# Optimization experiments

Measured on AMD Instinct MI355X. Metric: run time of the kernel, lower is better.

The kernel has to match this reference:

```python
import jax, jax.numpy as jnp
import numpy as np

B = 65536
G = 9          # grid_size
C = 10         # num_classes
BS = 3         # block_size = sqrt(grid_size)
CONSTRAINT_WEIGHT = 0.1


def setup_inputs() -> dict:
    key = jax.random.key(0)
    k1, k2, k3 = jax.random.split(key, 3)
    logits = jax.random.normal(k1, (B, G, G, C), dtype=jnp.float32)
    targets = jax.random.randint(k2, (B, G, G), 0, C)
    puzzles = jax.random.randint(k3, (B, G, G), 0, C)
    return {"logits": logits, "targets": targets, "puzzles": puzzles}


def _sudoku_loss(logits, targets, puzzles):
    mask = (puzzles == 0).astype(logits.dtype)               # [B, G, G]

    # --- masked cross-entropy over empty cells ---
    logp = jax.nn.log_softmax(logits, axis=-1)               # [B, G, G, C]
    ce = -jnp.take_along_axis(logp, targets[..., None], axis=-1)[..., 0]
    ce_loss = (ce * mask).sum() / (mask.sum() + 1e-8)

    # --- constraint loss (rows, cols, 3x3 boxes), fully vectorized ---
    probs = jnp.exp(logp)                                    # softmax probs
    wp = probs * mask[..., None]                             # [B, G, G, C]

    def group_mse(digit_sums, msum):
        # digit_sums: [B, G_groups, C]; msum: [B, G_groups]
        # torch: per-group F.mse_loss over [B, C-1], summed over groups
        target = msum[..., None] / G                         # [B, Gg, 1]
        diff = digit_sums[..., 1:] - target                  # [B, Gg, C-1]
        return (diff * diff).mean(axis=(0, 2)).sum()

    # rows: sum over columns (axis 2)
    row_loss = group_mse(wp.sum(axis=2), mask.sum(axis=2))
    # cols: sum over rows (axis 1)
    col_loss = group_mse(wp.sum(axis=1), mask.sum(axis=1))
    # boxes: reshape to [B, bi, ri, bj, cj, C], sum within-box dims
    box_ds = wp.reshape(B, BS, BS, BS, BS, C).sum(axis=(2, 4)).reshape(B, G, C)
    box_ms = mask.reshape(B, BS, BS, BS, BS).sum(axis=(2, 4)).reshape(B, G)
    box_loss = group_mse(box_ds, box_ms)

    num_constraints = G * 2 + BS * BS                        # 27
    constraint_loss = (row_loss + col_loss + box_loss) / num_constraints

    # torch wraps the constraint loss in torch.tensor(...), detaching it
    total = ce_loss + CONSTRAINT_WEIGHT * jax.lax.stop_gradient(constraint_loss)
    return total, ce_loss, constraint_loss


def reference(logits, targets, puzzles):
    total, ce_loss, constraint_loss = _sudoku_loss(logits, targets, puzzles)
    return total, ce_loss, constraint_loss
```

## Files before the change

### kernel.cpp

```cpp
#include <hip/hip_runtime.h>


constexpr int kB     = 65536;
constexpr int TPB    = 512;
constexpr int NBLK   = 1024;
constexpr int PPBLK  = kB / NBLK;
constexpr int PPB_R  = 6;
constexpr int ROUNDS = (PPBLK + PPB_R - 1) / PPB_R;
constexpr int NSLOT  = 256;
constexpr int SLOT_STRIDE = 16;
constexpr int CSTRIDE = 12;

__global__ __launch_bounds__(TPB, 8) void sudoku_main(
    const float* __restrict__ logits,
    const int*   __restrict__ targets,
    const int*   __restrict__ puzzles,
    float*       __restrict__ ws)
{
    __shared__ __align__(16) float probs[TPB * CSTRIDE];
    __shared__ float red[3][TPB / 64];

    const int  tid  = threadIdx.x;
    const int  q    = tid / 81;
    const bool actq = (q < PPB_R);
    const size_t blkbase = (size_t)blockIdx.x * PPBLK * 81;

    float ce = 0.f, mcnt = 0.f, diff2 = 0.f;

    int pz_cur = 1;
    if (actq) pz_cur = puzzles[blkbase + tid];

    for (int r = 0; r < ROUNDS; ++r) {
        int pz_next = 1;
        if (r + 1 < ROUNDS) {
            const bool actn = actq && ((r + 1) * PPB_R + q < PPBLK);
            if (actn) pz_next = puzzles[blkbase + (size_t)(r + 1) * (PPB_R * 81) + tid];
        }

        const bool act = actq && (r * PPB_R + q < PPBLK);
        float wv[10];
        #pragma unroll
        for (int c = 0; c < 10; ++c) wv[c] = 0.f;

        if (act && pz_cur == 0) {
            const size_t idx = blkbase + (size_t)r * (PPB_R * 81) + tid;
            const int tg = targets[idx];
            const float* xp = logits + idx * 10;
            float2 v0 = *(const float2*)(xp + 0);
            float2 v1 = *(const float2*)(xp + 2);
            float2 v2 = *(const float2*)(xp + 4);
            float2 v3 = *(const float2*)(xp + 6);
            float2 v4 = *(const float2*)(xp + 8);
            float x[10];
            x[0]=v0.x; x[1]=v0.y; x[2]=v1.x; x[3]=v1.y; x[4]=v2.x;
            x[5]=v2.y; x[6]=v3.x; x[7]=v3.y; x[8]=v4.x; x[9]=v4.y;

            float mx = x[0];
            #pragma unroll
            for (int c = 1; c < 10; ++c) mx = fmaxf(mx, x[c]);
            float e[10];
            float S = 0.f;
            #pragma unroll
            for (int c = 0; c < 10; ++c) { e[c] = __expf(x[c] - mx); S += e[c]; }
            const float inv = 1.0f / S;

            float xt = x[0];
            #pragma unroll
            for (int c = 1; c < 10; ++c) xt = (tg == c) ? x[c] : xt;
            ce   += mx + __logf(S) - xt;
            mcnt += 1.f;
            wv[0] = 1.f;
            #pragma unroll
            for (int c = 1; c < 10; ++c) wv[c] = e[c] * inv;
        }

        {
            float* dst = &probs[tid * CSTRIDE];
            *(float4*)(dst + 0) = make_float4(wv[0], wv[1], wv[2], wv[3]);
            *(float4*)(dst + 4) = make_float4(wv[4], wv[5], wv[6], wv[7]);
            *(float2*)(dst + 8) = make_float2(wv[8], wv[9]);
        }
        __syncthreads();

        if (tid < PPB_R * 27) {
            float s[10];
            #pragma unroll
            for (int c = 0; c < 10; ++c) s[c] = 0.f;

            if (tid < PPB_R * 9) {
                const int q2 = tid / 9, rr = tid - q2 * 9;
                const float* base = &probs[(q2 * 81 + rr * 9) * CSTRIDE];
                #pragma unroll
                for (int i = 0; i < 9; ++i) {
                    const float* cell = base + i * CSTRIDE;
                    const float4 a = *(const float4*)(cell + 0);
                    const float4 b = *(const float4*)(cell + 4);
                    const float2 c2 = *(const float2*)(cell + 8);
                    s[0]+=a.x; s[1]+=a.y; s[2]+=a.z; s[3]+=a.w;
                    s[4]+=b.x; s[5]+=b.y; s[6]+=b.z; s[7]+=b.w;
                    s[8]+=c2.x; s[9]+=c2.y;
                }
            } else if (tid < PPB_R * 18) {
                const int u = tid - PPB_R * 9;
                const int q2 = u / 9, j = u - q2 * 9;
                const float* base = &probs[(q2 * 81 + j) * CSTRIDE];
                #pragma unroll
                for (int i = 0; i < 9; ++i) {
                    const float* cell = base + i * (9 * CSTRIDE);
                    const float4 a = *(const float4*)(cell + 0);
                    const float4 b = *(const float4*)(cell + 4);
                    const float2 c2 = *(const float2*)(cell + 8);
                    s[0]+=a.x; s[1]+=a.y; s[2]+=a.z; s[3]+=a.w;
                    s[4]+=b.x; s[5]+=b.y; s[6]+=b.z; s[7]+=b.w;
                    s[8]+=c2.x; s[9]+=c2.y;
                }
            } else {
                const int u = tid - PPB_R * 18;
                const int q2 = u / 9, b = u - q2 * 9;
                const int br = b / 3, bc = b - br * 3;
                const float* base = &probs[(q2 * 81 + br * 27 + bc * 3) * CSTRIDE];
                #pragma unroll
                for (int dr = 0; dr < 3; ++dr) {
                    #pragma unroll
                    for (int dc = 0; dc < 3; ++dc) {
                        const float* cell = base + (dr * 9 + dc) * CSTRIDE;
                        const float4 a = *(const float4*)(cell + 0);
                        const float4 bb = *(const float4*)(cell + 4);
                        const float2 c2 = *(const float2*)(cell + 8);
                        s[0]+=a.x; s[1]+=a.y; s[2]+=a.z; s[3]+=a.w;
                        s[4]+=bb.x; s[5]+=bb.y; s[6]+=bb.z; s[7]+=bb.w;
                        s[8]+=c2.x; s[9]+=c2.y;
                    }
                }
            }
            const float tm = s[0] * (1.f / 9.f);
            #pragma unroll
            for (int c = 1; c < 10; ++c) { const float d = s[c] - tm; diff2 += d * d; }
        }
        __syncthreads();

        pz_cur = pz_next;
    }

    #pragma unroll
    for (int off = 32; off > 0; off >>= 1) {
        diff2 += __shfl_down(diff2, off);
        ce    += __shfl_down(ce, off);
        mcnt  += __shfl_down(mcnt, off);
    }
    const int wave = tid >> 6;
    if ((tid & 63) == 0) { red[0][wave] = diff2; red[1][wave] = ce; red[2][wave] = mcnt; }
    __syncthreads();
    if (tid == 0) {
        float d = 0.f, c2 = 0.f, m = 0.f;
        #pragma unroll
        for (int w = 0; w < TPB / 64; ++w) { d += red[0][w]; c2 += red[1][w]; m += red[2][w]; }
        float* slot = ws + (size_t)(blockIdx.x & (NSLOT - 1)) * SLOT_STRIDE;
        atomicAdd(&slot[0], d);
        atomicAdd(&slot[1], c2);
        atomicAdd(&slot[2], m);
    }
}

__global__ void sudoku_final(const float* __restrict__ ws, float* __restrict__ out)
{
    const int t = threadIdx.x;
    float d = 0.f, c2 = 0.f, m = 0.f;
    for (int s = t; s < NSLOT; s += 64) {
        const float* sl = ws + (size_t)s * SLOT_STRIDE;
        d += sl[0]; c2 += sl[1]; m += sl[2];
    }
    #pragma unroll
    for (int off = 32; off > 0; off >>= 1) {
        d  += __shfl_down(d, off);
        c2 += __shfl_down(c2, off);
        m  += __shfl_down(m, off);
    }
    if (t == 0) {
        const float ce_loss = c2 / (m + 1e-8f);
        const float constraint = d / ((float)kB * 9.f * 27.f);
        out[0] = ce_loss + 0.1f * constraint;
        out[1] = ce_loss;
        out[2] = constraint;
    }
}

extern "C" void kernel_launch(void* const* d_in, const int* in_sizes, int n_in,
                              void* d_out, int out_size, void* d_ws, size_t ws_size,
                              hipStream_t stream)
{
    const float* logits  = (const float*)d_in[0];
    const int*   targets = (const int*)d_in[1];
    const int*   puzzles = (const int*)d_in[2];
    float* ws  = (float*)d_ws;
    float* out = (float*)d_out;

    hipMemsetAsync(d_ws, 0, NSLOT * SLOT_STRIDE * sizeof(float), stream);

    sudoku_main<<<NBLK, TPB, 0, stream>>>(logits, targets, puzzles, ws);
    sudoku_final<<<1, 64, 0, stream>>>(ws, out);
}
```

Measured before the change: 295.7 us.

## Overlap global logit loads with previous round's group reductions

```diff
diff --git a/kernel.cpp b/kernel.cpp
--- a/kernel.cpp
+++ b/kernel.cpp
@@ -11,6 +11,67 @@
 constexpr int SLOT_STRIDE = 16;
 constexpr int CSTRIDE = 12;
 
+__device__ __forceinline__ float group_mse(const float* __restrict__ probs, int tid)
+{
+    float diff2 = 0.f;
+    if (tid < PPB_R * 27) {
+        float s[10];
+        #pragma unroll
+        for (int c = 0; c < 10; ++c) s[c] = 0.f;
+
+        if (tid < PPB_R * 9) {
+            const int q2 = tid / 9, rr = tid - q2 * 9;
+            const float* base = &probs[(q2 * 81 + rr * 9) * CSTRIDE];
+            #pragma unroll
+            for (int i = 0; i < 9; ++i) {
+                const float* cell = base + i * CSTRIDE;
+                const float4 a = *(const float4*)(cell + 0);
+                const float4 b = *(const float4*)(cell + 4);
+                const float2 c2 = *(const float2*)(cell + 8);
+                s[0]+=a.x; s[1]+=a.y; s[2]+=a.z; s[3]+=a.w;
+                s[4]+=b.x; s[5]+=b.y; s[6]+=b.z; s[7]+=b.w;
+                s[8]+=c2.x; s[9]+=c2.y;
+            }
+        } else if (tid < PPB_R * 18) {
+            const int u = tid - PPB_R * 9;
+            const int q2 = u / 9, j = u - q2 * 9;
+            const float* base = &probs[(q2 * 81 + j) * CSTRIDE];
+            #pragma unroll
+            for (int i = 0; i < 9; ++i) {
+                const float* cell = base + i * (9 * CSTRIDE);
+                const float4 a = *(const float4*)(cell + 0);
+                const float4 b = *(const float4*)(cell + 4);
+                const float2 c2 = *(const float2*)(cell + 8);
+                s[0]+=a.x; s[1]+=a.y; s[2]+=a.z; s[3]+=a.w;
+                s[4]+=b.x; s[5]+=b.y; s[6]+=b.z; s[7]+=b.w;
+                s[8]+=c2.x; s[9]+=c2.y;
+            }
+        } else {
+            const int u = tid - PPB_R * 18;
+            const int q2 = u / 9, b = u - q2 * 9;
+            const int br = b / 3, bc = b - br * 3;
+            const float* base = &probs[(q2 * 81 + br * 27 + bc * 3) * CSTRIDE];
+            #pragma unroll
+            for (int dr = 0; dr < 3; ++dr) {
+                #pragma unroll
+                for (int dc = 0; dc < 3; ++dc) {
+                    const float* cell = base + (dr * 9 + dc) * CSTRIDE;
+                    const float4 a = *(const float4*)(cell + 0);
+                    const float4 bb = *(const float4*)(cell + 4);
+                    const float2 c2 = *(const float2*)(cell + 8);
+                    s[0]+=a.x; s[1]+=a.y; s[2]+=a.z; s[3]+=a.w;
+                    s[4]+=bb.x; s[5]+=bb.y; s[6]+=bb.z; s[7]+=bb.w;
+                    s[8]+=c2.x; s[9]+=c2.y;
+                }
+            }
+        }
+        const float tm = s[0] * (1.f / 9.f);
+        #pragma unroll
+        for (int c = 1; c < 10; ++c) { const float d = s[c] - tm; diff2 += d * d; }
+    }
+    return diff2;
+}
+
 __global__ __launch_bounds__(TPB, 8) void sudoku_main(
     const float* __restrict__ logits,
     const int*   __restrict__ targets,
@@ -31,30 +92,36 @@
     if (actq) pz_cur = puzzles[blkbase + tid];
 
     for (int r = 0; r < ROUNDS; ++r) {
+        const bool act = actq && (r * PPB_R + q < PPBLK);
+        const bool m   = act && (pz_cur == 0);
+
+        int tg = 0;
+        float2 g0 = make_float2(0.f, 0.f), g1 = g0, g2 = g0, g3 = g0, g4 = g0;
+        if (m) {
+            const size_t idx = blkbase + (size_t)r * (PPB_R * 81) + tid;
+            tg = targets[idx];
+            const float* xp = logits + idx * 10;
+            g0 = *(const float2*)(xp + 0);
+            g1 = *(const float2*)(xp + 2);
+            g2 = *(const float2*)(xp + 4);
+            g3 = *(const float2*)(xp + 6);
+            g4 = *(const float2*)(xp + 8);
+        }
         int pz_next = 1;
         if (r + 1 < ROUNDS) {
             const bool actn = actq && ((r + 1) * PPB_R + q < PPBLK);
             if (actn) pz_next = puzzles[blkbase + (size_t)(r + 1) * (PPB_R * 81) + tid];
         }
 
-        const bool act = actq && (r * PPB_R + q < PPBLK);
+        if (r > 0) diff2 += group_mse(probs, tid);
+
         float wv[10];
         #pragma unroll
         for (int c = 0; c < 10; ++c) wv[c] = 0.f;
-
-        if (act && pz_cur == 0) {
-            const size_t idx = blkbase + (size_t)r * (PPB_R * 81) + tid;
-            const int tg = targets[idx];
-            const float* xp = logits + idx * 10;
-            float2 v0 = *(const float2*)(xp + 0);
-            float2 v1 = *(const float2*)(xp + 2);
-            float2 v2 = *(const float2*)(xp + 4);
-            float2 v3 = *(const float2*)(xp + 6);
-            float2 v4 = *(const float2*)(xp + 8);
+        if (m) {
             float x[10];
-            x[0]=v0.x; x[1]=v0.y; x[2]=v1.x; x[3]=v1.y; x[4]=v2.x;
-            x[5]=v2.y; x[6]=v3.x; x[7]=v3.y; x[8]=v4.x; x[9]=v4.y;
-
+            x[0]=g0.x; x[1]=g0.y; x[2]=g1.x; x[3]=g1.y; x[4]=g2.x;
+            x[5]=g2.y; x[6]=g3.x; x[7]=g3.y; x[8]=g4.x; x[9]=g4.y;
             float mx = x[0];
             #pragma unroll
             for (int c = 1; c < 10; ++c) mx = fmaxf(mx, x[c]);
@@ -63,7 +130,6 @@
             #pragma unroll
             for (int c = 0; c < 10; ++c) { e[c] = __expf(x[c] - mx); S += e[c]; }
             const float inv = 1.0f / S;
-
             float xt = x[0];
             #pragma unroll
             for (int c = 1; c < 10; ++c) xt = (tg == c) ? x[c] : xt;
@@ -73,6 +139,8 @@
             #pragma unroll
             for (int c = 1; c < 10; ++c) wv[c] = e[c] * inv;
         }
+
+        __syncthreads();
 
         {
             float* dst = &probs[tid * CSTRIDE];
@@ -82,65 +150,9 @@
         }
         __syncthreads();
 
-        if (tid < PPB_R * 27) {
-            float s[10];
-            #pragma unroll
-            for (int c = 0; c < 10; ++c) s[c] = 0.f;
-
-            if (tid < PPB_R * 9) {
-                const int q2 = tid / 9, rr = tid - q2 * 9;
-                const float* base = &probs[(q2 * 81 + rr * 9) * CSTRIDE];
-                #pragma unroll
-                for (int i = 0; i < 9; ++i) {
-                    const float* cell = base + i * CSTRIDE;
-                    const float4 a = *(const float4*)(cell + 0);
-                    const float4 b = *(const float4*)(cell + 4);
-                    const float2 c2 = *(const float2*)(cell + 8);
-                    s[0]+=a.x; s[1]+=a.y; s[2]+=a.z; s[3]+=a.w;
-                    s[4]+=b.x; s[5]+=b.y; s[6]+=b.z; s[7]+=b.w;
-                    s[8]+=c2.x; s[9]+=c2.y;
-                }
-            } else if (tid < PPB_R * 18) {
-                const int u = tid - PPB_R * 9;
-                const int q2 = u / 9, j = u - q2 * 9;
-                const float* base = &probs[(q2 * 81 + j) * CSTRIDE];
-                #pragma unroll
-                for (int i = 0; i < 9; ++i) {
-                    const float* cell = base + i * (9 * CSTRIDE);
-                    const float4 a = *(const float4*)(cell + 0);
-                    const float4 b = *(const float4*)(cell + 4);
-                    const float2 c2 = *(const float2*)(cell + 8);
-                    s[0]+=a.x; s[1]+=a.y; s[2]+=a.z; s[3]+=a.w;
-                    s[4]+=b.x; s[5]+=b.y; s[6]+=b.z; s[7]+=b.w;
-                    s[8]+=c2.x; s[9]+=c2.y;
-                }
-            } else {
-                const int u = tid - PPB_R * 18;
-                const int q2 = u / 9, b = u - q2 * 9;
-                const int br = b / 3, bc = b - br * 3;
-                const float* base = &probs[(q2 * 81 + br * 27 + bc * 3) * CSTRIDE];
-                #pragma unroll
-                for (int dr = 0; dr < 3; ++dr) {
-                    #pragma unroll
-                    for (int dc = 0; dc < 3; ++dc) {
-                        const float* cell = base + (dr * 9 + dc) * CSTRIDE;
-                        const float4 a = *(const float4*)(cell + 0);
-                        const float4 bb = *(const float4*)(cell + 4);
-                        const float2 c2 = *(const float2*)(cell + 8);
-                        s[0]+=a.x; s[1]+=a.y; s[2]+=a.z; s[3]+=a.w;
-                        s[4]+=bb.x; s[5]+=bb.y; s[6]+=bb.z; s[7]+=bb.w;
-                        s[8]+=c2.x; s[9]+=c2.y;
-                    }
-                }
-            }
-            const float tm = s[0] * (1.f / 9.f);
-            #pragma unroll
-            for (int c = 1; c < 10; ++c) { const float d = s[c] - tm; diff2 += d * d; }
-        }
-        __syncthreads();
-
         pz_cur = pz_next;
     }
+    diff2 += group_mse(probs, tid);
 
     #pragma unroll
     for (int off = 32; off > 0; off >>= 1) {
```

Measured after the change: 643.0 us. 2.17x slower.
